# Optimization experiments

Hardware: AMD Instinct MI355X
Metric: run time of the kernel (lower is better)

Reference implementation:

```python
import jax, jax.numpy as jnp
import numpy as np

B, DIM, HEADS, H, W = 4, 64, 8, 512, 512


def _conv(x, w, groups=1):
    # NCHW x, OIHW w, stride 1, SAME padding (padding=k//2 in torch)
    return jax.lax.conv_general_dilated(
        x, w, (1, 1), 'SAME', feature_group_count=groups,
        dimension_numbers=('NCHW', 'OIHW', 'NCHW'))


def _dwt_haar(x):
    # single-level orthonormal haar on even-sized NCHW input
    a = x[..., 0::2, 0::2]; b = x[..., 0::2, 1::2]
    c = x[..., 1::2, 0::2]; d = x[..., 1::2, 1::2]
    LL = (a + b + c + d) * 0.5
    LH = (-a - b + c + d) * 0.5
    HL = (-a + b - c + d) * 0.5
    HH = (a - b - c + d) * 0.5
    return LL, LH, HL, HH


def _idwt_haar(LL, LH, HL, HH):
    a = (LL - LH - HL + HH) * 0.5
    b = (LL - LH + HL - HH) * 0.5
    c = (LL + LH - HL - HH) * 0.5
    d = (LL + LH + HL + HH) * 0.5
    Bn, C, h, w = LL.shape
    even = jnp.stack([a, b], -1).reshape(Bn, C, h, 2 * w)  # rows 0::2
    odd = jnp.stack([c, d], -1).reshape(Bn, C, h, 2 * w)   # rows 1::2
    return jnp.stack([even, odd], -2).reshape(Bn, C, 2 * h, 2 * w)


def _l2norm(x, eps=1e-12):
    n = jnp.sqrt(jnp.sum(x * x, axis=-1, keepdims=True))
    return x / jnp.maximum(n, eps)


def setup_inputs() -> dict:
    key = jax.random.key(0)
    ks = jax.random.split(key, 8)
    def w(k, shape):
        fan_in = shape[1] * shape[2] * shape[3]
        return jax.random.normal(k, shape, jnp.float32) * (1.0 / np.sqrt(fan_in))
    return {
        'x': jax.random.normal(ks[0], (B, DIM, H, W), jnp.float32),
        'w_hc1': w(ks[1], (2 * DIM, DIM, 3, 3)),        # groups=2 over 2*dim channels
        'w_hc2': w(ks[2], (DIM, 2 * DIM, 1, 1)),
        'w_ho': w(ks[3], (3 * DIM, DIM, 3, 3)),          # groups=3 over 3*dim channels
        'w_qkv': w(ks[4], (3 * DIM, DIM, 1, 1)),
        'w_dw': w(ks[5], (3 * DIM, 1, 3, 3)),            # depthwise, groups=3*dim
        'w_proj': w(ks[6], (DIM, DIM, 1, 1)),
        'temperature': jnp.ones((HEADS, 1, 1), jnp.float32),
    }


def reference(x, w_hc1, w_hc2, w_ho, w_qkv, w_dw, w_proj, temperature):
    LL, LH, HL, HH = _dwt_haar(x)

    # high-frequency (LH,HL) filter branch
    hv = jnp.concatenate([LH, HL], axis=1)
    filter_hv = jax.nn.relu(_conv(jax.nn.relu(_conv(hv, w_hc1, groups=2)), w_hc2))

    # qkv from LL: 1x1 conv then depthwise 3x3
    qkv = _conv(_conv(LL, w_qkv), w_dw, groups=3 * DIM)
    q, k, v = jnp.split(qkv, 3, axis=1)
    b, c, h, w = q.shape
    v = v * filter_hv + v

    ch = c // HEADS
    q = q.reshape(b, HEADS, ch, h * w)
    k = k.reshape(b, HEADS, ch, h * w)
    v = v.reshape(b, HEADS, ch, h * w)
    q = _l2norm(q)
    k = _l2norm(k)

    attn = jnp.einsum('bhcn,bhdn->bhcd', q, k) * temperature  # [b,heads,ch,ch]
    attn = jax.nn.softmax(attn, axis=-1)
    out = jnp.einsum('bhcd,bhdn->bhcn', attn, v).reshape(b, c, h, w)
    out = _conv(out, w_proj)

    # high-frequency output branch
    yh = jax.nn.relu(_conv(jnp.concatenate([LH, HL, HH], axis=1), w_ho, groups=3))
    LH2, HL2, HH2 = jnp.split(yh, 3, axis=1)

    return _idwt_haar(out, LH2, HL2, HH2)
```

## Files before the change

kernel.cpp:

```cpp
#include <hip/hip_runtime.h>
#include <hip/hip_bf16.h>

#define BN 4
#define DIM 64
#define NHEADS 8
#define HH 256
#define WH 256
#define NP (HH*WH)
#define HF 512
#define WF 512

#define PD 258
#define PROW (PD*64)
#define PPLANE ((size_t)PD*PD*64)

typedef __attribute__((ext_vector_type(8))) short bfx8;
typedef __attribute__((ext_vector_type(8))) unsigned short u16x8;
typedef __attribute__((ext_vector_type(4))) float f32x4;

static __device__ __forceinline__ short f2bf(float f) {
    unsigned u = __float_as_uint(f);
    unsigned r = (u + 0x7FFFu + ((u >> 16) & 1u)) >> 16;
    return (short)r;
}
static __device__ __forceinline__ float bfu(unsigned short u) {
    return __uint_as_float((unsigned)u << 16);
}

__global__ __launch_bounds__(256) void k_setup(unsigned short* __restrict__ tiled16,
                                               const float* __restrict__ w_ho,
                                               const float* __restrict__ w_hc1,
                                               const float* __restrict__ w_hc2,
                                               const float* __restrict__ w_qkv,
                                               short* __restrict__ wrHO,
                                               short* __restrict__ wrHC1,
                                               short* __restrict__ wrHC2,
                                               short* __restrict__ wrQKV) {
    int bx = blockIdx.x, tid = threadIdx.x;
    if (bx < 16) {
        char* base = (char*)(tiled16 + (size_t)bx * PPLANE);
        const int ROWB = PROW * 2;
        for (int k = tid; k < 8224; k += 256) {
            char* dst;
            if (k < 2064) dst = base + (size_t)k * 16;
            else if (k < 4128) dst = base + (size_t)257 * ROWB + (size_t)(k - 2064) * 16;
            else if (k < 6176) { int r = (k - 4128) >> 3, s = (k - 4128) & 7;
                dst = base + (size_t)(r + 1) * ROWB + (size_t)s * 16; }
            else { int r = (k - 6176) >> 3, s = (k - 6176) & 7;
                dst = base + (size_t)(r + 1) * ROWB + 257 * 128 + (size_t)s * 16; }
            *(uint4*)dst = (uint4){0, 0, 0, 0};
        }
        return;
    }
    if (bx < 16 + 432 + 288) {
        const float* w = (bx < 448) ? w_ho : w_hc1;
        short* wrep = (bx < 448) ? wrHO : wrHC1;
        int t = (bx - ((bx < 448) ? 16 : 448)) * 256 + tid;
        unsigned g   = (unsigned)t / 36864u;
        unsigned r1  = (unsigned)t % 36864u;
        unsigned tap = r1 / 4096u;
        unsigned r2  = r1 % 4096u;
        unsigned icb = r2 / 512u;
        unsigned r3  = r2 % 512u;
        unsigned oc  = r3 >> 3;
        unsigned j   = r3 & 7u;
        wrep[t] = f2bf(w[(((size_t)g * 64 + oc) * 64 + icb * 8u + j) * 9 + tap]);
        return;
    }
    if (bx < 16 + 432 + 288 + 32) {
        int t = (bx - 736) * 256 + tid;
        int j = t & 7, gr = t >> 3, o16 = gr & 15, X = gr >> 4;
        int icb = X % 16, oct = X / 16;
        wrHC2[t] = f2bf(w_hc2[(size_t)(oct * 16 + o16) * 128 + icb * 8 + j]);
        return;
    }
    {
        int t = (bx - 768) * 256 + tid;
        int j = t & 7, gr = t >> 3, o16 = gr & 15, X = gr >> 4;
        int icb = X % 8, oct = X / 8;
        wrQKV[t] = f2bf(w_qkv[(size_t)(oct * 16 + o16) * 64 + icb * 8 + j]);
    }
}

__global__ __launch_bounds__(256) void k_dwt(const float* __restrict__ x,
                                             unsigned short* __restrict__ tiled,
                                             unsigned short* __restrict__ llp) {
    __shared__ unsigned short lds[3 * 128 * 64] __attribute__((aligned(16)));
    const int tid = threadIdx.x;
    const int pid = blockIdx.x;
    const int b = blockIdx.y;
    const int y0 = (pid >> 4) * 8, x0 = (pid & 15) * 16;
    const int quad = tid & 127;
    const int qy = quad >> 4, qx = quad & 15;
    const int gy = y0 + qy, gx = x0 + qx;
    const int ich = tid >> 7;
    unsigned short* llb = llp + (size_t)b * PPLANE + ((size_t)(gy + 1) * PD + (gx + 1)) * 64;

#pragma unroll 4
    for (int it = 0; it < 16; ++it) {
        int ic = it * 4 + ich * 2;
        unsigned g = (((unsigned)(ic >> 3)) + (unsigned)gx + 2u * (unsigned)gy) & 7u;
        unsigned swz = (unsigned)quad * 64 + (g << 3) + (unsigned)(ic & 7);
        unsigned pk[3], pll;
#pragma unroll
        for (int s = 0; s < 2; ++s) {
            const float* px = x + (((size_t)(b * 64 + ic + s) * HF) + 2 * gy) * WF + 2 * gx;
            float2 e0 = *(const float2*)px;
            float2 e1 = *(const float2*)(px + WF);
            float a = e0.x, bb = e0.y, c = e1.x, d = e1.y;
            unsigned ll = (unsigned short)f2bf(( a + bb + c + d) * 0.5f);
            unsigned lh = (unsigned short)f2bf((-a - bb + c + d) * 0.5f);
            unsigned hl = (unsigned short)f2bf((-a + bb - c + d) * 0.5f);
            unsigned hh = (unsigned short)f2bf(( a - bb - c + d) * 0.5f);
            if (s == 0) { pll = ll; pk[0] = lh; pk[1] = hl; pk[2] = hh; }
            else { pll |= ll << 16; pk[0] |= lh << 16; pk[1] |= hl << 16; pk[2] |= hh << 16; }
        }
        *(unsigned*)&lds[swz]          = pk[0];
        *(unsigned*)&lds[8192 + swz]   = pk[1];
        *(unsigned*)&lds[16384 + swz]  = pk[2];
        *(unsigned*)&llb[(g << 3) + (unsigned)(ic & 7)] = pll;
    }
    __syncthreads();
#pragma unroll
    for (int it = 0; it < 12; ++it) {
        int cch = tid + it * 256;
        int p = cch >> 10, rem = cch & 1023;
        int row = rem >> 7, col = rem & 127;
        unsigned short* dst = tiled + ((size_t)(b * 3 + p) * PD + (y0 + row + 1)) * PROW
                                    + (size_t)(x0 + 1) * 64 + (size_t)col * 8;
        *(uint4*)dst = *(const uint4*)((const char*)lds + (size_t)cch * 16);
    }
}

template <int LAYOUT>
__global__ __launch_bounds__(256) void k_gconv3x3_mfma(const unsigned short* __restrict__ tiled,
                                                       const bfx8* __restrict__ wr,
                                                       unsigned short* __restrict__ out, int OC) {
    __shared__ short lds_in[324 * 64] __attribute__((aligned(16)));
    const int tid = threadIdx.x;
    const int l = tid & 63, wv = tid >> 6;
    const int tile = blockIdx.x;
    const int x0 = (tile & 15) * 16, y0 = (tile >> 4) * 16;
    const int g = blockIdx.y, b = blockIdx.z;
    const unsigned short* src = tiled + (size_t)(b * 3 + g) * PPLANE;

#pragma unroll
    for (int it = 0; it < 10; ++it) {
        int cch = it * 256 + tid;
        unsigned row = (unsigned)cch / 144u, col = (unsigned)cch % 144u;
        const unsigned short* ga = src + (size_t)(y0 + row) * PROW + (size_t)x0 * 64 + (size_t)col * 8;
        __builtin_amdgcn_global_load_lds(
            (const __attribute__((address_space(1))) void*)ga,
            (__attribute__((address_space(3))) void*)((char*)lds_in + (size_t)(it * 256 + wv * 64) * 16),
            16, 0, 0);
    }
    if (tid < 32) {
        int cch = 2560 + tid;
        unsigned row = (unsigned)cch / 144u, col = (unsigned)cch % 144u;
        const unsigned short* ga = src + (size_t)(y0 + row) * PROW + (size_t)x0 * 64 + (size_t)col * 8;
        *(uint4*)((char*)lds_in + (size_t)cch * 16) = *(const uint4*)ga;
    }
    __syncthreads();

    f32x4 acc[4][4];
#pragma unroll
    for (int i = 0; i < 4; ++i)
#pragma unroll
        for (int j = 0; j < 4; ++j) acc[i][j] = (f32x4){0.f, 0.f, 0.f, 0.f};

    const int lx = l & 15, lq = l >> 4;
#pragma unroll
    for (int c = 0; c < 2; ++c) {
        const int icb = c * 4 + lq;
#pragma unroll
        for (int tap = 0; tap < 9; ++tap) {
            const int dy = tap / 3, dx = tap % 3;
            const size_t wbase = ((size_t)(g * 9 + tap) * 8 + icb) * 64 + lx;
            bfx8 b0 = wr[wbase];
            bfx8 b1 = wr[wbase + 16];
            bfx8 b2 = wr[wbase + 32];
            bfx8 b3 = wr[wbase + 48];
#pragma unroll
            for (int pg = 0; pg < 4; ++pg) {
                int hy = wv * 4 + pg + dy, hx = lx + dx;
                int hp = hy * 18 + hx;
                const bfx8* ap = (const bfx8*)&lds_in[hp * 64 + (((icb + hx + 2 * hy + 5) & 7) << 3)];
                bfx8 a = *ap;
                acc[pg][0] = __builtin_amdgcn_mfma_f32_16x16x32_bf16(a, b0, acc[pg][0], 0, 0, 0);
                acc[pg][1] = __builtin_amdgcn_mfma_f32_16x16x32_bf16(a, b1, acc[pg][1], 0, 0, 0);
                acc[pg][2] = __builtin_amdgcn_mfma_f32_16x16x32_bf16(a, b2, acc[pg][2], 0, 0, 0);
                acc[pg][3] = __builtin_amdgcn_mfma_f32_16x16x32_bf16(a, b3, acc[pg][3], 0, 0, 0);
            }
        }
    }

#pragma unroll
    for (int pg = 0; pg < 4; ++pg) {
#pragma unroll
        for (int ocg = 0; ocg < 4; ++ocg) {
            f32x4 v = acc[pg][ocg];
            if (LAYOUT == 0) {
                unsigned short* op = out + ((size_t)b * OC + g * 64 + ocg * 16 + lx) * NP
                                         + (size_t)(y0 + wv * 4 + pg) * WH + x0 + lq * 4;
                ushort4 s4;
                s4.x = (unsigned short)f2bf(fmaxf(v.x, 0.f));
                s4.y = (unsigned short)f2bf(fmaxf(v.y, 0.f));
                s4.z = (unsigned short)f2bf(fmaxf(v.z, 0.f));
                s4.w = (unsigned short)f2bf(fmaxf(v.w, 0.f));
                *(ushort4*)op = s4;
            } else {
                int icT = g * 64 + ocg * 16 + lx;
                int g16 = icT >> 3;
                unsigned short* tb = out + ((size_t)(b * 256 + tile) * 256) * 128;
                int innerb = (wv * 4 + pg) * 16 + lq * 4;
                float vr[4] = {v.x, v.y, v.z, v.w};
#pragma unroll
                for (int r = 0; r < 4; ++r) {
                    int inn = innerb + r;
                    tb[(size_t)inn * 128 + (((g16 + inn) & 15) << 3) + (icT & 7)] =
                        (unsigned short)f2bf(fmaxf(vr[r], 0.f));
                }
            }
        }
    }
}

template <int CIN, int OC, bool RELU>
__global__ __launch_bounds__(256) void k_conv1x1_mfma(const unsigned short* __restrict__ inT,
                                                      const bfx8* __restrict__ wr,
                                                      unsigned short* __restrict__ out) {
    constexpr int KB = CIN / 8;
    constexpr int KC = CIN / 32;
    constexpr int NOCT = OC / 16;
    __shared__ short ldsA[256 * CIN] __attribute__((aligned(16)));
    const int tid = threadIdx.x;
    const int l = tid & 63, wv = tid >> 6;
    const int tile = blockIdx.x, b = blockIdx.y;
    const unsigned short* src = inT + ((size_t)(b * 256 + tile) * 256) * CIN;
    constexpr int ITER = (256 * CIN / 8) / 256;
#pragma unroll
    for (int it = 0; it < ITER; ++it) {
        int cc = it * 256 + tid;
        __builtin_amdgcn_global_load_lds(
            (const __attribute__((address_space(1))) void*)(src + (size_t)cc * 8),
            (__attribute__((address_space(3))) void*)((char*)ldsA + (size_t)(it * 256 + wv * 64) * 16),
            16, 0, 0);
    }
    __syncthreads();

    const int lx = l & 15, lq = l >> 4;
    const int x0 = (tile & 15) * 16, y0 = (tile >> 4) * 16;
#pragma unroll
    for (int o4 = 0; o4 < NOCT / 4; ++o4) {
        f32x4 acc[4][4];
#pragma unroll
        for (int i = 0; i < 4; ++i)
#pragma unroll
            for (int j = 0; j < 4; ++j) acc[i][j] = (f32x4){0.f, 0.f, 0.f, 0.f};
#pragma unroll
        for (int c = 0; c < KC; ++c) {
            const int icb = c * 4 + lq;
            bfx8 bf[4];
#pragma unroll
            for (int ot = 0; ot < 4; ++ot)
                bf[ot] = wr[(size_t)(((o4 * 4 + ot) * KB + icb) * 16) + lx];
#pragma unroll
            for (int pg = 0; pg < 4; ++pg) {
                int inner = (wv * 4 + pg) * 16 + lx;
                const bfx8* ap = (const bfx8*)&ldsA[inner * CIN + (((icb + inner) & (KB - 1)) << 3)];
                bfx8 a = *ap;
                acc[pg][0] = __builtin_amdgcn_mfma_f32_16x16x32_bf16(a, bf[0], acc[pg][0], 0, 0, 0);
                acc[pg][1] = __builtin_amdgcn_mfma_f32_16x16x32_bf16(a, bf[1], acc[pg][1], 0, 0, 0);
                acc[pg][2] = __builtin_amdgcn_mfma_f32_16x16x32_bf16(a, bf[2], acc[pg][2], 0, 0, 0);
                acc[pg][3] = __builtin_amdgcn_mfma_f32_16x16x32_bf16(a, bf[3], acc[pg][3], 0, 0, 0);
            }
        }
#pragma unroll
        for (int pg = 0; pg < 4; ++pg)
#pragma unroll
            for (int ot = 0; ot < 4; ++ot) {
                int oc = (o4 * 4 + ot) * 16 + lx;
                unsigned short* op = out + ((size_t)b * OC + oc) * NP
                                         + (size_t)(y0 + wv * 4 + pg) * WH + x0 + lq * 4;
                f32x4 v = acc[pg][ot];
                ushort4 s4;
                s4.x = (unsigned short)f2bf(RELU ? fmaxf(v.x, 0.f) : v.x);
                s4.y = (unsigned short)f2bf(RELU ? fmaxf(v.y, 0.f) : v.y);
                s4.z = (unsigned short)f2bf(RELU ? fmaxf(v.z, 0.f) : v.z);
                s4.w = (unsigned short)f2bf(RELU ? fmaxf(v.w, 0.f) : v.w);
                *(ushort4*)op = s4;
            }
    }
}

__global__ __launch_bounds__(256) void k_qkv_fused(const unsigned short* __restrict__ llp,
                                                   const bfx8* __restrict__ wrq,
                                                   const float* __restrict__ wdw,
                                                   const unsigned short* __restrict__ filt,
                                                   unsigned short* __restrict__ qkv) {
    __shared__ short ldsA[336 * 64] __attribute__((aligned(16)));
    __shared__ float ldsW[192 * 9];
    const int tid = threadIdx.x;
    const int l = tid & 63, wv = tid >> 6;
    const int tile = blockIdx.x, b = blockIdx.y;
    const int x0 = (tile & 15) * 16, y0 = (tile >> 4) * 16;
    const unsigned short* src = llp + (size_t)b * PPLANE;

#pragma unroll
    for (int it = 0; it < 10; ++it) {
        int cch = it * 256 + tid;
        unsigned row = (unsigned)cch / 144u, col = (unsigned)cch % 144u;
        const unsigned short* ga = src + (size_t)(y0 + row) * PROW + (size_t)x0 * 64 + (size_t)col * 8;
        __builtin_amdgcn_global_load_lds(
            (const __attribute__((address_space(1))) void*)ga,
            (__attribute__((address_space(3))) void*)((char*)ldsA + (size_t)(it * 256 + wv * 64) * 16),
            16, 0, 0);
    }
    if (tid < 32) {
        int cch = 2560 + tid;
        unsigned row = (unsigned)cch / 144u, col = (unsigned)cch % 144u;
        const unsigned short* ga = src + (size_t)(y0 + row) * PROW + (size_t)x0 * 64 + (size_t)col * 8;
        *(uint4*)((char*)ldsA + (size_t)cch * 16) = *(const uint4*)ga;
    }
    for (int k = tid; k < 1728; k += 256) ldsW[k] = wdw[k];
    __syncthreads();

    const int lx = l & 15, lq = l >> 4;
    bfx8 af[6][2];
#pragma unroll
    for (int m = 0; m < 6; ++m) {
        int mt = wv + 4 * m;
        if (mt < 21) {
            int hp = mt * 16 + lx;
            int hy = hp / 18, hx = hp - hy * 18;
#pragma unroll
            for (int kc = 0; kc < 2; ++kc) {
                int icb = kc * 4 + lq;
                af[m][kc] = *(const bfx8*)&ldsA[hp * 64 + (((icb + hx + 2 * hy + 5) & 7) << 3)];
            }
        }
    }
    __syncthreads();

    for (int g3 = 0; g3 < 3; ++g3) {
        bfx8 bw[2][4];
#pragma unroll
        for (int kc = 0; kc < 2; ++kc)
#pragma unroll
            for (int nt = 0; nt < 4; ++nt)
                bw[kc][nt] = wrq[(size_t)(((g3 * 4 + nt) * 8) + kc * 4 + lq) * 16 + lx];
#pragma unroll
        for (int m = 0; m < 6; ++m) {
            int mt = wv + 4 * m;
            if (mt < 21) {
                f32x4 acc[4];
#pragma unroll
                for (int nt = 0; nt < 4; ++nt) acc[nt] = (f32x4){0.f, 0.f, 0.f, 0.f};
#pragma unroll
                for (int kc = 0; kc < 2; ++kc) {
                    bfx8 a = af[m][kc];
#pragma unroll
                    for (int nt = 0; nt < 4; ++nt)
                        acc[nt] = __builtin_amdgcn_mfma_f32_16x16x32_bf16(a, bw[kc][nt], acc[nt], 0, 0, 0);
                }
#pragma unroll
                for (int nt = 0; nt < 4; ++nt) {
                    int ocl = nt * 16 + lx;
                    float vr[4] = {acc[nt].x, acc[nt].y, acc[nt].z, acc[nt].w};
#pragma unroll
                    for (int r = 0; r < 4; ++r) {
                        int hp2 = mt * 16 + lq * 4 + r;
                        int hy2 = hp2 / 18, hx2 = hp2 - hy2 * 18;
                        ldsA[hp2 * 64 + ((((ocl >> 3) + hx2 + 2 * hy2) & 7) << 3) + (ocl & 7)] =
                            f2bf(vr[r]);
                    }
                }
            }
        }
        __syncthreads();
        {
            const int ch = l, chg = g3 * 64 + ch;
            float w9[9];
#pragma unroll
            for (int t = 0; t < 9; ++t) w9[t] = ldsW[chg * 9 + t];
#pragma unroll
            for (int yy = 0; yy < 4; ++yy) {
                int y = wv * 4 + yy;
                float ln[3][18];
#pragma unroll
                for (int hr = 0; hr < 3; ++hr) {
                    int hy = y + hr;
#pragma unroll
                    for (int hx = 0; hx < 18; ++hx)
                        ln[hr][hx] = bfu((unsigned short)ldsA[(hy * 18 + hx) * 64 +
                                         ((((ch >> 3) + hx + 2 * hy) & 7) << 3) + (ch & 7)]);
                }
                float ox[16];
#pragma unroll
                for (int xx = 0; xx < 16; ++xx) {
                    float s = 0.f;
#pragma unroll
                    for (int hr = 0; hr < 3; ++hr)
#pragma unroll
                        for (int dx = 0; dx < 3; ++dx)
                            s = fmaf(ln[hr][xx + dx], w9[hr * 3 + dx], s);
                    ox[xx] = s;
                }
                if (g3 == 2) {
                    const unsigned short* fp = filt + ((size_t)b * 64 + ch) * NP
                                                    + (size_t)(y0 + y) * WH + x0;
                    u16x8 f0 = *(const u16x8*)fp;
                    u16x8 f1 = *(const u16x8*)(fp + 8);
#pragma unroll
                    for (int k = 0; k < 8; ++k) ox[k]     = fmaf(ox[k],     bfu(f0[k]), ox[k]);
#pragma unroll
                    for (int k = 0; k < 8; ++k) ox[8 + k] = fmaf(ox[8 + k], bfu(f1[k]), ox[8 + k]);
                }
                u16x8 s0, s1;
#pragma unroll
                for (int k = 0; k < 8; ++k) { s0[k] = (unsigned short)f2bf(ox[k]);
                                              s1[k] = (unsigned short)f2bf(ox[8 + k]); }
                unsigned short* op = qkv + ((size_t)b * 192 + chg) * NP + (size_t)(y0 + y) * WH + x0;
                *(u16x8*)op = s0;
                *(u16x8*)(op + 8) = s1;
            }
        }
        __syncthreads();
    }
}

__global__ __launch_bounds__(256) void k_attn_dot(const unsigned short* __restrict__ qkv,
                                                  float* __restrict__ praw,
                                                  float* __restrict__ praw2) {
    int bhd = blockIdx.x, sp = blockIdx.y;
    int b = bhd >> 3, hd = bhd & 7;
    const unsigned short* qb = qkv + ((size_t)b * 192 + hd * 8) * NP;
    const unsigned short* kb = qkv + ((size_t)b * 192 + 64 + hd * 8) * NP;
    float acc[64], acc2[16];
#pragma unroll
    for (int i = 0; i < 64; ++i) acc[i] = 0.f;
#pragma unroll
    for (int i = 0; i < 16; ++i) acc2[i] = 0.f;
    int n0 = sp * (NP / 8);
    for (int n = n0 + threadIdx.x; n < n0 + NP / 8; n += 256) {
        float qv[8], kv[8];
#pragma unroll
        for (int c2 = 0; c2 < 8; ++c2) qv[c2] = bfu(qb[(size_t)c2 * NP + n]);
#pragma unroll
        for (int d2 = 0; d2 < 8; ++d2) kv[d2] = bfu(kb[(size_t)d2 * NP + n]);
#pragma unroll
        for (int c2 = 0; c2 < 8; ++c2) {
            acc2[c2] = fmaf(qv[c2], qv[c2], acc2[c2]);
#pragma unroll
            for (int d2 = 0; d2 < 8; ++d2)
                acc[c2 * 8 + d2] = fmaf(qv[c2], kv[d2], acc[c2 * 8 + d2]);
        }
#pragma unroll
        for (int d2 = 0; d2 < 8; ++d2) acc2[8 + d2] = fmaf(kv[d2], kv[d2], acc2[8 + d2]);
    }
    __shared__ float red[4][64];
#pragma unroll
    for (int i = 0; i < 64; ++i) {
        float v = acc[i];
#pragma unroll
        for (int off = 32; off; off >>= 1) v += __shfl_down(v, off);
        if ((threadIdx.x & 63) == 0) red[threadIdx.x >> 6][i] = v;
    }
    __syncthreads();
    if (threadIdx.x < 64)
        praw[((size_t)sp * 32 + bhd) * 64 + threadIdx.x] =
            red[0][threadIdx.x] + red[1][threadIdx.x] + red[2][threadIdx.x] + red[3][threadIdx.x];
    __syncthreads();
#pragma unroll
    for (int i = 0; i < 16; ++i) {
        float v = acc2[i];
#pragma unroll
        for (int off = 32; off; off >>= 1) v += __shfl_down(v, off);
        if ((threadIdx.x & 63) == 0) red[threadIdx.x >> 6][i] = v;
    }
    __syncthreads();
    if (threadIdx.x < 16)
        praw2[((size_t)sp * 32 + bhd) * 16 + threadIdx.x] =
            red[0][threadIdx.x] + red[1][threadIdx.x] + red[2][threadIdx.x] + red[3][threadIdx.x];
}

__global__ __launch_bounds__(64) void k_attn_soft(const float* __restrict__ praw,
                                                  const float* __restrict__ praw2,
                                                  const float* __restrict__ temp,
                                                  float* __restrict__ attn) {
    int bhd = blockIdx.x;
    int hd = bhd & 7;
    int t = threadIdx.x, c = t >> 3, d = t & 7;
    float s = 0.f, sq = 0.f, sk = 0.f;
    for (int sp = 0; sp < 8; ++sp) {
        s  += praw[((size_t)sp * 32 + bhd) * 64 + t];
        sq += praw2[((size_t)sp * 32 + bhd) * 16 + c];
        sk += praw2[((size_t)sp * 32 + bhd) * 16 + 8 + d];
    }
    float nq = fmaxf(sqrtf(sq), 1e-12f);
    float nk = fmaxf(sqrtf(sk), 1e-12f);
    s = s / (nq * nk) * temp[hd];
    __shared__ float sm[64];
    __shared__ float se[64];
    sm[t] = s;
    __syncthreads();
    float mx = -1e30f;
#pragma unroll
    for (int dd = 0; dd < 8; ++dd) mx = fmaxf(mx, sm[c * 8 + dd]);
    float e = __expf(s - mx);
    se[t] = e;
    __syncthreads();
    float sum = 0.f;
#pragma unroll
    for (int dd = 0; dd < 8; ++dd) sum += se[c * 8 + dd];
    attn[(size_t)bhd * 64 + t] = e / sum;
}

__global__ __launch_bounds__(256) void k_attnout_idwt(const unsigned short* __restrict__ qkv,
                                                      const float* __restrict__ attn,
                                                      const float* __restrict__ wproj,
                                                      const unsigned short* __restrict__ yh,
                                                      float* __restrict__ out) {
    __shared__ float wsh[64 * 64];
    __shared__ float ash[512];
    const int tid = threadIdx.x;
    const int b = blockIdx.y;
    const int p = blockIdx.x * 256 + tid;
#pragma unroll
    for (int it = 0; it < 16; ++it) wsh[tid + it * 256] = wproj[tid + it * 256];
#pragma unroll
    for (int it = 0; it < 2; ++it) ash[tid + it * 256] = attn[(size_t)b * 512 + tid + it * 256];
    __syncthreads();

    float av[64];
    const unsigned short* vb = qkv + ((size_t)b * 192 + 128) * NP + p;
#pragma unroll
    for (int hd = 0; hd < 8; ++hd) {
        float vv[8];
#pragma unroll
        for (int d = 0; d < 8; ++d) vv[d] = bfu(vb[(size_t)(hd * 8 + d) * NP]);
#pragma unroll
        for (int c2 = 0; c2 < 8; ++c2) {
            float s = 0.f;
#pragma unroll
            for (int d = 0; d < 8; ++d) s = fmaf(ash[hd * 64 + c2 * 8 + d], vv[d], s);
            av[hd * 8 + c2] = s;
        }
    }
    const int i = p >> 8, j = p & 255;
    const unsigned short* yb = yh + (size_t)b * 192 * NP + p;
    float* ob = out + ((size_t)b * 64 * HF + 2 * i) * WF + 2 * j;
    for (int c = 0; c < 64; ++c) {
        float s = 0.f;
#pragma unroll
        for (int ic = 0; ic < 64; ++ic) s = fmaf(av[ic], wsh[c * 64 + ic], s);
        float LHv = bfu(yb[(size_t)c * NP]);
        float HLv = bfu(yb[(size_t)(c + 64) * NP]);
        float HHv = bfu(yb[(size_t)(c + 128) * NP]);
        float* oc_ = ob + (size_t)c * HF * WF;
        *(float2*)oc_        = make_float2((s - LHv - HLv + HHv) * 0.5f, (s - LHv + HLv - HHv) * 0.5f);
        *(float2*)(oc_ + WF) = make_float2((s + LHv - HLv - HHv) * 0.5f, (s + LHv + HLv + HHv) * 0.5f);
    }
}

extern "C" void kernel_launch(void* const* d_in, const int* in_sizes, int n_in,
                              void* d_out, int out_size, void* d_ws, size_t ws_size,
                              hipStream_t stream) {
    const float* x      = (const float*)d_in[0];
    const float* w_hc1  = (const float*)d_in[1];
    const float* w_hc2  = (const float*)d_in[2];
    const float* w_ho   = (const float*)d_in[3];
    const float* w_qkv  = (const float*)d_in[4];
    const float* w_dw   = (const float*)d_in[5];
    const float* w_proj = (const float*)d_in[6];
    const float* temp   = (const float*)d_in[7];
    float* out = (float*)d_out;

    char* base = (char*)d_ws;
    unsigned short* TILED = (unsigned short*)(base + 0);
    unsigned short* LLP   = (unsigned short*)(base + 102242304ULL);
    unsigned short* YH    = (unsigned short*)(base + 136323072ULL);
    unsigned short* T1T   = (unsigned short*)(base + 236986368ULL);
    unsigned short* FILT  = (unsigned short*)(base + 304095232ULL);
    unsigned short* QKV   = (unsigned short*)(base + 337649664ULL);
    float*          PRAW  = (float*)(base + 438312960ULL);
    float*          PRAW2 = (float*)(base + 438378496ULL);
    float*          ATTN  = (float*)(base + 438394880ULL);
    short* WREP_HO  = (short*)(base + 438403072ULL);
    short* WREP_HC1 = (short*)(base + 438624256ULL);
    short* WREP_HC2 = (short*)(base + 438771712ULL);
    short* WREP_QKV = (short*)(base + 438788096ULL);

    k_setup<<<816, 256, 0, stream>>>(TILED, w_ho, w_hc1, w_hc2, w_qkv,
                                     WREP_HO, WREP_HC1, WREP_HC2, WREP_QKV);
    k_dwt<<<dim3(512, BN), 256, 0, stream>>>(x, TILED, LLP);
    k_gconv3x3_mfma<0><<<dim3(256, 3, BN), 256, 0, stream>>>(TILED, (const bfx8*)WREP_HO, YH, 192);
    k_gconv3x3_mfma<1><<<dim3(256, 2, BN), 256, 0, stream>>>(TILED, (const bfx8*)WREP_HC1, T1T, 128);
    k_conv1x1_mfma<128, 64, true><<<dim3(256, BN), 256, 0, stream>>>(T1T, (const bfx8*)WREP_HC2, FILT);
    k_qkv_fused<<<dim3(256, BN), 256, 0, stream>>>(LLP, (const bfx8*)WREP_QKV, w_dw, FILT, QKV);
    k_attn_dot<<<dim3(32, 8), 256, 0, stream>>>(QKV, PRAW, PRAW2);
    k_attn_soft<<<32, 64, 0, stream>>>(PRAW, PRAW2, temp, ATTN);
    k_attnout_idwt<<<dim3(256, BN), 256, 0, stream>>>(QKV, ATTN, w_proj, YH, out);
}
```

Before: 613.5 us.

## Fold attention into projection matrix and run output stage on MFMA with tiled YH

Precomputes per-batch combined matrix Wproj·blockdiag(attn) in bf16 in a new small kernel, so the output kernel does one 64x64 MFMA matmul per pixel tile instead of scalar FP32 attention-apply plus projection. The high-frequency conv output is now written in a per-tile layout so the IDWT stage reads contiguous vectors and writes float4 rows. The attention dot kernel also switches to 8-wide vectorized bf16 loads. Adds bf16 rounding of the folded matrix and an extra launch.

```diff
diff --git a/kernel.cpp b/kernel.cpp
--- a/kernel.cpp
+++ b/kernel.cpp
@@ -16,6 +16,7 @@
 
 typedef __attribute__((ext_vector_type(8))) short bfx8;
 typedef __attribute__((ext_vector_type(8))) unsigned short u16x8;
+typedef __attribute__((ext_vector_type(4))) unsigned short u16x4;
 typedef __attribute__((ext_vector_type(4))) float f32x4;
 
 static __device__ __forceinline__ short f2bf(float f) {
@@ -200,8 +201,8 @@
         for (int ocg = 0; ocg < 4; ++ocg) {
             f32x4 v = acc[pg][ocg];
             if (LAYOUT == 0) {
-                unsigned short* op = out + ((size_t)b * OC + g * 64 + ocg * 16 + lx) * NP
-                                         + (size_t)(y0 + wv * 4 + pg) * WH + x0 + lq * 4;
+                unsigned short* op = out + ((size_t)(b * 256 + tile) * OC + g * 64 + ocg * 16 + lx) * 256
+                                         + (wv * 4 + pg) * 16 + lq * 4;
                 ushort4 s4;
                 s4.x = (unsigned short)f2bf(fmaxf(v.x, 0.f));
                 s4.y = (unsigned short)f2bf(fmaxf(v.y, 0.f));
@@ -442,21 +443,31 @@
 #pragma unroll
     for (int i = 0; i < 16; ++i) acc2[i] = 0.f;
     int n0 = sp * (NP / 8);
-    for (int n = n0 + threadIdx.x; n < n0 + NP / 8; n += 256) {
-        float qv[8], kv[8];
-#pragma unroll
-        for (int c2 = 0; c2 < 8; ++c2) qv[c2] = bfu(qb[(size_t)c2 * NP + n]);
-#pragma unroll
-        for (int d2 = 0; d2 < 8; ++d2) kv[d2] = bfu(kb[(size_t)d2 * NP + n]);
-#pragma unroll
-        for (int c2 = 0; c2 < 8; ++c2) {
-            acc2[c2] = fmaf(qv[c2], qv[c2], acc2[c2]);
-#pragma unroll
-            for (int d2 = 0; d2 < 8; ++d2)
-                acc[c2 * 8 + d2] = fmaf(qv[c2], kv[d2], acc[c2 * 8 + d2]);
-        }
-#pragma unroll
-        for (int d2 = 0; d2 < 8; ++d2) acc2[8 + d2] = fmaf(kv[d2], kv[d2], acc2[8 + d2]);
+#pragma unroll 2
+    for (int it = 0; it < 4; ++it) {
+        int n = n0 + (it * 256 + threadIdx.x) * 8;
+        u16x8 q8[8], k8[8];
+#pragma unroll
+        for (int c2 = 0; c2 < 8; ++c2) q8[c2] = *(const u16x8*)(qb + (size_t)c2 * NP + n);
+#pragma unroll
+        for (int d2 = 0; d2 < 8; ++d2) k8[d2] = *(const u16x8*)(kb + (size_t)d2 * NP + n);
+#pragma unroll
+        for (int j = 0; j < 8; ++j) {
+            float qv[8], kv[8];
+#pragma unroll
+            for (int c2 = 0; c2 < 8; ++c2) qv[c2] = bfu(q8[c2][j]);
+#pragma unroll
+            for (int d2 = 0; d2 < 8; ++d2) kv[d2] = bfu(k8[d2][j]);
+#pragma unroll
+            for (int c2 = 0; c2 < 8; ++c2) {
+                acc2[c2] = fmaf(qv[c2], qv[c2], acc2[c2]);
+#pragma unroll
+                for (int d2 = 0; d2 < 8; ++d2)
+                    acc[c2 * 8 + d2] = fmaf(qv[c2], kv[d2], acc[c2 * 8 + d2]);
+            }
+#pragma unroll
+            for (int d2 = 0; d2 < 8; ++d2) acc2[8 + d2] = fmaf(kv[d2], kv[d2], acc2[8 + d2]);
+        }
     }
     __shared__ float red[4][64];
 #pragma unroll
@@ -516,50 +527,88 @@
     attn[(size_t)bhd * 64 + t] = e / sum;
 }
 
+__global__ __launch_bounds__(256) void k_prep_attn(const float* __restrict__ attn,
+                                                   const float* __restrict__ wproj,
+                                                   short* __restrict__ mrep) {
+    int b = blockIdx.x, t = threadIdx.x;
+    const float* ab = attn + (size_t)b * 512;
+#pragma unroll
+    for (int i = 0; i < 16; ++i) {
+        int idx = t * 16 + i;
+        int j = idx & 7, o16 = (idx >> 3) & 15, icb = (idx >> 7) & 7, oct = idx >> 10;
+        int oc = oct * 16 + o16;
+        float m = 0.f;
+#pragma unroll
+        for (int c8 = 0; c8 < 8; ++c8)
+            m = fmaf(wproj[(size_t)oc * 64 + icb * 8 + c8], ab[icb * 64 + c8 * 8 + j], m);
+        mrep[(size_t)b * 4096 + idx] = f2bf(m);
+    }
+}
+
 __global__ __launch_bounds__(256) void k_attnout_idwt(const unsigned short* __restrict__ qkv,
-                                                      const float* __restrict__ attn,
-                                                      const float* __restrict__ wproj,
-                                                      const unsigned short* __restrict__ yh,
+                                                      const bfx8* __restrict__ mrep,
+                                                      const unsigned short* __restrict__ yht,
                                                       float* __restrict__ out) {
-    __shared__ float wsh[64 * 64];
-    __shared__ float ash[512];
     const int tid = threadIdx.x;
-    const int b = blockIdx.y;
-    const int p = blockIdx.x * 256 + tid;
-#pragma unroll
-    for (int it = 0; it < 16; ++it) wsh[tid + it * 256] = wproj[tid + it * 256];
-#pragma unroll
-    for (int it = 0; it < 2; ++it) ash[tid + it * 256] = attn[(size_t)b * 512 + tid + it * 256];
-    __syncthreads();
-
-    float av[64];
-    const unsigned short* vb = qkv + ((size_t)b * 192 + 128) * NP + p;
-#pragma unroll
-    for (int hd = 0; hd < 8; ++hd) {
-        float vv[8];
-#pragma unroll
-        for (int d = 0; d < 8; ++d) vv[d] = bfu(vb[(size_t)(hd * 8 + d) * NP]);
-#pragma unroll
-        for (int c2 = 0; c2 < 8; ++c2) {
-            float s = 0.f;
-#pragma unroll
-            for (int d = 0; d < 8; ++d) s = fmaf(ash[hd * 64 + c2 * 8 + d], vv[d], s);
-            av[hd * 8 + c2] = s;
-        }
-    }
-    const int i = p >> 8, j = p & 255;
-    const unsigned short* yb = yh + (size_t)b * 192 * NP + p;
-    float* ob = out + ((size_t)b * 64 * HF + 2 * i) * WF + 2 * j;
-    for (int c = 0; c < 64; ++c) {
-        float s = 0.f;
-#pragma unroll
-        for (int ic = 0; ic < 64; ++ic) s = fmaf(av[ic], wsh[c * 64 + ic], s);
-        float LHv = bfu(yb[(size_t)c * NP]);
-        float HLv = bfu(yb[(size_t)(c + 64) * NP]);
-        float HHv = bfu(yb[(size_t)(c + 128) * NP]);
-        float* oc_ = ob + (size_t)c * HF * WF;
-        *(float2*)oc_        = make_float2((s - LHv - HLv + HHv) * 0.5f, (s - LHv + HLv - HHv) * 0.5f);
-        *(float2*)(oc_ + WF) = make_float2((s + LHv - HLv - HHv) * 0.5f, (s + LHv + HLv + HHv) * 0.5f);
+    const int l = tid & 63, wv = tid >> 6;
+    const int lx = l & 15, lq = l >> 4;
+    const int tile = blockIdx.x, b = blockIdx.y;
+    const int x0 = (tile & 15) * 16, y0 = (tile >> 4) * 16;
+    const unsigned short* vb = qkv + ((size_t)b * 192 + 128) * NP;
+    const bfx8* mb = mrep + (size_t)b * 512;
+
+    bfx8 bw[2][4];
+#pragma unroll
+    for (int kc = 0; kc < 2; ++kc)
+#pragma unroll
+        for (int nt = 0; nt < 4; ++nt)
+            bw[kc][nt] = mb[(nt * 8 + kc * 4 + lq) * 16 + lx];
+
+    const unsigned short* yb = yht + (size_t)(b * 256 + tile) * 192 * 256;
+
+#pragma unroll
+    for (int pg = 0; pg < 4; ++pg) {
+        const int mt = wv * 4 + pg;
+        const int y = y0 + mt;
+        const unsigned short* vrow = vb + (size_t)y * WH + x0 + lx;
+        bfx8 a0, a1;
+#pragma unroll
+        for (int j = 0; j < 8; ++j) a0[j] = (short)vrow[(size_t)(lq * 8 + j) * NP];
+#pragma unroll
+        for (int j = 0; j < 8; ++j) a1[j] = (short)vrow[(size_t)(32 + lq * 8 + j) * NP];
+
+        f32x4 acc[4];
+#pragma unroll
+        for (int nt = 0; nt < 4; ++nt) acc[nt] = (f32x4){0.f, 0.f, 0.f, 0.f};
+#pragma unroll
+        for (int nt = 0; nt < 4; ++nt) {
+            acc[nt] = __builtin_amdgcn_mfma_f32_16x16x32_bf16(a0, bw[0][nt], acc[nt], 0, 0, 0);
+            acc[nt] = __builtin_amdgcn_mfma_f32_16x16x32_bf16(a1, bw[1][nt], acc[nt], 0, 0, 0);
+        }
+#pragma unroll
+        for (int nt = 0; nt < 4; ++nt) {
+            const int oc = nt * 16 + lx;
+            const int inner = mt * 16 + lq * 4;
+            const unsigned short* yp = yb + (size_t)oc * 256 + inner;
+            u16x4 lh4 = *(const u16x4*)yp;
+            u16x4 hl4 = *(const u16x4*)(yp + (size_t)64 * 256);
+            u16x4 hh4 = *(const u16x4*)(yp + (size_t)128 * 256);
+            float e0[8], e1[8];
+#pragma unroll
+            for (int r = 0; r < 4; ++r) {
+                float s  = acc[nt][r];
+                float LH = bfu(lh4[r]), HL = bfu(hl4[r]), HHv = bfu(hh4[r]);
+                e0[2 * r]     = (s - LH - HL + HHv) * 0.5f;
+                e0[2 * r + 1] = (s - LH + HL - HHv) * 0.5f;
+                e1[2 * r]     = (s + LH - HL - HHv) * 0.5f;
+                e1[2 * r + 1] = (s + LH + HL + HHv) * 0.5f;
+            }
+            float* o0 = out + ((size_t)(b * 64 + oc) * HF + 2 * y) * WF + 2 * (x0 + lq * 4);
+            *(float4*)o0            = *(float4*)&e0[0];
+            *(float4*)(o0 + 4)      = *(float4*)&e0[4];
+            *(float4*)(o0 + WF)     = *(float4*)&e1[0];
+            *(float4*)(o0 + WF + 4) = *(float4*)&e1[4];
+        }
     }
 }
 
@@ -590,6 +639,7 @@
     short* WREP_HC1 = (short*)(base + 438624256ULL);
     short* WREP_HC2 = (short*)(base + 438771712ULL);
     short* WREP_QKV = (short*)(base + 438788096ULL);
+    short* MREP     = (short*)(base + 438812672ULL);
 
     k_setup<<<816, 256, 0, stream>>>(TILED, w_ho, w_hc1, w_hc2, w_qkv,
                                      WREP_HO, WREP_HC1, WREP_HC2, WREP_QKV);
@@ -600,5 +650,6 @@
     k_qkv_fused<<<dim3(256, BN), 256, 0, stream>>>(LLP, (const bfx8*)WREP_QKV, w_dw, FILT, QKV);
     k_attn_dot<<<dim3(32, 8), 256, 0, stream>>>(QKV, PRAW, PRAW2);
     k_attn_soft<<<32, 64, 0, stream>>>(PRAW, PRAW2, temp, ATTN);
-    k_attnout_idwt<<<dim3(256, BN), 256, 0, stream>>>(QKV, ATTN, w_proj, YH, out);
-}
+    k_prep_attn<<<BN, 256, 0, stream>>>(ATTN, w_proj, MREP);
+    k_attnout_idwt<<<dim3(256, BN), 256, 0, stream>>>(QKV, (const bfx8*)MREP, YH, out);
+}
```

Result: no change. 602.9 us (-1.7%).
